# Optimization experiments

Hardware: AMD Instinct MI355X
Metric: run time of the kernel (lower is better)

Reference implementation:

```python
import jax, jax.numpy as jnp
import numpy as np

D_MODEL = 512
B, T = 2, 4096
LN_EPS = 1e-5


def _layernorm(x, gamma, beta):
    mu = jnp.mean(x, axis=-1, keepdims=True)
    var = jnp.mean((x - mu) ** 2, axis=-1, keepdims=True)
    return (x - mu) * jax.lax.rsqrt(var + LN_EPS) * gamma + beta


def setup_inputs() -> dict:
    key = jax.random.key(0)
    ks = jax.random.split(key, 16)
    d = D_MODEL
    s = 1.0 / np.sqrt(d)
    inp = {
        "tokens": jax.random.normal(ks[0], (B, T, d), dtype=jnp.float32),
        "Wq": jax.random.normal(ks[1], (d, d), dtype=jnp.float32) * s,
        "bq": jnp.zeros((d,), jnp.float32),
        "Wk": jax.random.normal(ks[2], (d, d), dtype=jnp.float32) * s,
        "bk": jnp.zeros((d,), jnp.float32),
        "Wv": jax.random.normal(ks[3], (d, d), dtype=jnp.float32) * s,
        "bv": jnp.zeros((d,), jnp.float32),
        "distance_scale": jnp.asarray(0.01, jnp.float32),
        "W1": jax.random.normal(ks[4], (d, 4 * d), dtype=jnp.float32) * s,
        "b1": jnp.zeros((4 * d,), jnp.float32),
        "W2": jax.random.normal(ks[5], (4 * d, d), dtype=jnp.float32) * (1.0 / np.sqrt(4 * d)),
        "b2": jnp.zeros((d,), jnp.float32),
        "g1": jnp.ones((d,), jnp.float32),
        "be1": jnp.zeros((d,), jnp.float32),
        "g2": jnp.ones((d,), jnp.float32),
        "be2": jnp.zeros((d,), jnp.float32),
    }
    return inp


def reference(tokens, Wq, bq, Wk, bk, Wv, bv, distance_scale,
              W1, b1, W2, b2, g1, be1, g2, be2):
    Bv, Tv, d = tokens.shape
    q = tokens @ Wq + bq
    k = tokens @ Wk + bk
    v = tokens @ Wv + bv
    # [B, T, T] raw scores
    scores = jnp.einsum('btd,bsd->bts', q, k)
    pos = jnp.arange(Tv)
    distance = jnp.abs(pos[None, :] - pos[:, None]).astype(jnp.float32)  # [T, T]
    scores = scores + (-distance_scale * distance)[None, :, :]
    causal = pos[None, :] > pos[:, None]  # strict upper triangle
    scores = jnp.where(causal[None, :, :], -jnp.inf, scores)
    scores = scores / jnp.sqrt(jnp.asarray(d, jnp.float32))
    attn = jax.nn.softmax(scores, axis=-1)
    attn_out = jnp.einsum('bts,bsd->btd', attn, v)
    x = _layernorm(tokens + attn_out, g1, be1)
    y = jnp.maximum(x @ W1 + b1, 0.0) @ W2 + b2
    z = _layernorm(y + x, g2, be2)
    return z
```

## Files before the change

kernel.cpp:

```cpp
#include <hip/hip_runtime.h>
#include <hip/hip_bf16.h>
#include <math.h>

typedef unsigned short u16;
typedef __attribute__((ext_vector_type(8))) short short8;
typedef __attribute__((ext_vector_type(4))) float float4v;

#define MFMA_BF16(a, b, c) __builtin_amdgcn_mfma_f32_16x16x32_bf16((a), (b), (c), 0, 0, 0)

typedef const __attribute__((address_space(1))) void* gas_ptr;
typedef __attribute__((address_space(3))) void* las_ptr;

__device__ __forceinline__ u16 f2bf(float f) {
  __hip_bfloat16 h = __float2bfloat16(f);
  return __builtin_bit_cast(u16, h);
}

__device__ __forceinline__ float bf2f(u16 v) {
  return __builtin_bit_cast(float, (unsigned)v << 16);
}

__device__ __forceinline__ void load_lds16(const u16* g, u16* l) {
  __builtin_amdgcn_global_load_lds((gas_ptr)g, (las_ptr)l, 16, 0, 0);
}

__device__ __forceinline__ void gemm_mainloop(
    const u16* __restrict__ A, const u16* __restrict__ Bt,
    int kb, int kend, int lda, int ldb,
    int m0, int n0, u16* As, u16* Bs, float4v acc[4][4])
{
  const int tid = threadIdx.x;
  const int w = tid >> 6, lane = tid & 63;
  const int wr = w >> 1, wc = w & 1;
  const int lr = lane & 15, lk = (lane >> 4) * 8;
  for (int k0 = kb; k0 < kend; k0 += 32) {
#pragma unroll
    for (int c = 0; c < 2; ++c) {
      int idx = c * 256 + w * 64 + lane;
      int r = idx >> 2, c8 = idx & 3;
      load_lds16(A + (size_t)(m0 + r) * lda + k0 + c8 * 8, As + (size_t)(c * 256 + w * 64) * 8);
      load_lds16(Bt + (size_t)(n0 + r) * ldb + k0 + c8 * 8, Bs + (size_t)(c * 256 + w * 64) * 8);
    }
    __syncthreads();
    short8 af[4], bf[4];
#pragma unroll
    for (int mt = 0; mt < 4; ++mt)
      af[mt] = *(const short8*)&As[(wr * 64 + mt * 16 + lr) * 32 + lk];
#pragma unroll
    for (int nt = 0; nt < 4; ++nt)
      bf[nt] = *(const short8*)&Bs[(wc * 64 + nt * 16 + lr) * 32 + lk];
#pragma unroll
    for (int mt = 0; mt < 4; ++mt)
#pragma unroll
      for (int nt = 0; nt < 4; ++nt)
        acc[mt][nt] = MFMA_BF16(af[mt], bf[nt], acc[mt][nt]);
    __syncthreads();
  }
}

__global__ __launch_bounds__(256) void gemm_qkv(
    const u16* __restrict__ A, const u16* __restrict__ Bt,
    const float* __restrict__ bq, const float* __restrict__ bk, const float* __restrict__ bv,
    u16* __restrict__ qo, u16* __restrict__ ko, u16* __restrict__ vto)
{
  __shared__ u16 As[128 * 32], Bs[128 * 32];
  float4v acc[4][4];
#pragma unroll
  for (int mt = 0; mt < 4; ++mt)
#pragma unroll
    for (int nt = 0; nt < 4; ++nt) acc[mt][nt] = (float4v){0.f, 0.f, 0.f, 0.f};
  const int m0 = blockIdx.y * 128, n0 = blockIdx.x * 128;
  gemm_mainloop(A, Bt, 0, 512, 512, 512, m0, n0, As, Bs, acc);
  const int tid = threadIdx.x, w = tid >> 6, lane = tid & 63;
  const int wr = w >> 1, wc = w & 1, lr = lane & 15, lg = lane >> 4;
#pragma unroll
  for (int mt = 0; mt < 4; ++mt) {
#pragma unroll
    for (int nt = 0; nt < 4; ++nt) {
      int n = n0 + wc * 64 + nt * 16 + lr;
#pragma unroll
      for (int r = 0; r < 4; ++r) {
        int i = m0 + wr * 64 + mt * 16 + lg * 4 + r;
        float v = acc[mt][nt][r];
        if (n < 512) {
          qo[(size_t)i * 512 + n] = f2bf(v + bq[n]);
        } else if (n < 1024) {
          ko[(size_t)i * 512 + (n - 512)] = f2bf(v + bk[n - 512]);
        } else {
          int bb = i >> 12, t = i & 4095;
          vto[((size_t)(bb * 512 + (n - 1024))) * 4096 + t] = f2bf(v + bv[n - 1024]);
        }
      }
    }
  }
}

__global__ __launch_bounds__(256) void gemm_qk_p(
    const u16* __restrict__ q, const u16* __restrict__ k,
    const float* __restrict__ dsp,
    u16* __restrict__ P, float* __restrict__ l)
{
  __shared__ u16 As[128 * 32], Bs[128 * 32];
  float4v acc[4][4];
#pragma unroll
  for (int mt = 0; mt < 4; ++mt)
#pragma unroll
    for (int nt = 0; nt < 4; ++nt) acc[mt][nt] = (float4v){0.f, 0.f, 0.f, 0.f};
  int idx = blockIdx.x;
  int tm = (int)((sqrtf(8.0f * (float)idx + 1.0f) - 1.0f) * 0.5f);
  while ((tm + 1) * (tm + 2) / 2 <= idx) ++tm;
  while (tm * (tm + 1) / 2 > idx) --tm;
  int tn = idx - tm * (tm + 1) / 2;
  const int m0 = tm * 128, n0 = tn * 128;
  gemm_mainloop(q, k, 0, 512, 512, 512, m0, n0, As, Bs, acc);
  const int tid = threadIdx.x, w = tid >> 6, lane = tid & 63;
  const int wr = w >> 1, wc = w & 1, lr = lane & 15, lg = lane >> 4;
  const float invs = 0.04419417382415922f;
  const float dsi = dsp[0] * invs;
  const float L2E = 1.4426950408889634f;
  float rs[4][4];
#pragma unroll
  for (int mt = 0; mt < 4; ++mt)
#pragma unroll
    for (int r = 0; r < 4; ++r) rs[mt][r] = 0.f;
#pragma unroll
  for (int mt = 0; mt < 4; ++mt) {
#pragma unroll
    for (int nt = 0; nt < 4; ++nt) {
      int j = n0 + wc * 64 + nt * 16 + lr;
#pragma unroll
      for (int r = 0; r < 4; ++r) {
        int i = m0 + wr * 64 + mt * 16 + lg * 4 + r;
        float x = acc[mt][nt][r] * invs - dsi * fabsf((float)(i - j));
        float p = (j > i) ? 0.f : exp2f(x * L2E);
        P[(size_t)i * 4096 + j] = f2bf(p);
        rs[mt][r] += p;
      }
    }
  }
#pragma unroll
  for (int mt = 0; mt < 4; ++mt) {
#pragma unroll
    for (int r = 0; r < 4; ++r) {
      float v = rs[mt][r];
#pragma unroll
      for (int off = 1; off < 16; off <<= 1) v += __shfl_xor(v, off, 64);
      if (lr == 0)
        atomicAdd(&l[m0 + wr * 64 + mt * 16 + lg * 4 + r], v);
    }
  }
}

__global__ __launch_bounds__(256) void gemm_pv(
    const u16* __restrict__ P, const u16* __restrict__ vt,
    float* __restrict__ of)
{
  __shared__ u16 As[128 * 32], Bs[128 * 32];
  float4v acc[4][4];
#pragma unroll
  for (int mt = 0; mt < 4; ++mt)
#pragma unroll
    for (int nt = 0; nt < 4; ++nt) acc[mt][nt] = (float4v){0.f, 0.f, 0.f, 0.f};
  int rem = blockIdx.y;
  int tm = 0, cpt = 1;
  while (rem >= cpt) { rem -= cpt; ++tm; cpt = (tm >> 3) + 1; }
  const int m0 = tm * 128, n0 = blockIdx.x * 128;
  const int kb = rem * 1024;
  const int kfull = (tm + 1) * 128;
  const int kend = (kb + 1024 < kfull) ? (kb + 1024) : kfull;
  gemm_mainloop(P, vt, kb, kend, 4096, 4096, m0, n0, As, Bs, acc);
  const int tid = threadIdx.x, w = tid >> 6, lane = tid & 63;
  const int wr = w >> 1, wc = w & 1, lr = lane & 15, lg = lane >> 4;
#pragma unroll
  for (int mt = 0; mt < 4; ++mt) {
#pragma unroll
    for (int nt = 0; nt < 4; ++nt) {
      int n = n0 + wc * 64 + nt * 16 + lr;
#pragma unroll
      for (int r = 0; r < 4; ++r) {
        int i = m0 + wr * 64 + mt * 16 + lg * 4 + r;
        atomicAdd(&of[(size_t)i * 512 + n], acc[mt][nt][r]);
      }
    }
  }
}

__global__ __launch_bounds__(256) void gemm_ffn1(
    const u16* __restrict__ A, const u16* __restrict__ Bt,
    const float* __restrict__ b1, u16* __restrict__ h)
{
  __shared__ u16 As[128 * 32], Bs[128 * 32];
  float4v acc[4][4];
#pragma unroll
  for (int mt = 0; mt < 4; ++mt)
#pragma unroll
    for (int nt = 0; nt < 4; ++nt) acc[mt][nt] = (float4v){0.f, 0.f, 0.f, 0.f};
  const int m0 = blockIdx.y * 128, n0 = blockIdx.x * 128;
  gemm_mainloop(A, Bt, 0, 512, 512, 512, m0, n0, As, Bs, acc);
  const int tid = threadIdx.x, w = tid >> 6, lane = tid & 63;
  const int wr = w >> 1, wc = w & 1, lr = lane & 15, lg = lane >> 4;
#pragma unroll
  for (int mt = 0; mt < 4; ++mt) {
#pragma unroll
    for (int nt = 0; nt < 4; ++nt) {
      int n = n0 + wc * 64 + nt * 16 + lr;
#pragma unroll
      for (int r = 0; r < 4; ++r) {
        int i = m0 + wr * 64 + mt * 16 + lg * 4 + r;
        h[(size_t)i * 2048 + n] = f2bf(fmaxf(acc[mt][nt][r] + b1[n], 0.f));
      }
    }
  }
}

__global__ __launch_bounds__(256) void gemm_ffn2(
    const u16* __restrict__ A, const u16* __restrict__ Bt,
    float* __restrict__ y0, u16* __restrict__ y1)
{
  __shared__ u16 As[128 * 32], Bs[128 * 32];
  float4v acc[4][4];
#pragma unroll
  for (int mt = 0; mt < 4; ++mt)
#pragma unroll
    for (int nt = 0; nt < 4; ++nt) acc[mt][nt] = (float4v){0.f, 0.f, 0.f, 0.f};
  const int m0 = blockIdx.y * 128, n0 = blockIdx.x * 128;
  const int kb = blockIdx.z * 1024;
  gemm_mainloop(A, Bt, kb, kb + 1024, 2048, 2048, m0, n0, As, Bs, acc);
  const int tid = threadIdx.x, w = tid >> 6, lane = tid & 63;
  const int wr = w >> 1, wc = w & 1, lr = lane & 15, lg = lane >> 4;
#pragma unroll
  for (int mt = 0; mt < 4; ++mt) {
#pragma unroll
    for (int nt = 0; nt < 4; ++nt) {
      int n = n0 + wc * 64 + nt * 16 + lr;
#pragma unroll
      for (int r = 0; r < 4; ++r) {
        int i = m0 + wr * 64 + mt * 16 + lg * 4 + r;
        if (blockIdx.z == 0) y0[(size_t)i * 512 + n] = acc[mt][nt][r];
        else                 y1[(size_t)i * 512 + n] = f2bf(acc[mt][nt][r]);
      }
    }
  }
}

__global__ __launch_bounds__(256) void ln1_kernel(
    const float* __restrict__ a, const float* __restrict__ lsum,
    const float* __restrict__ tok,
    const float* __restrict__ g, const float* __restrict__ be,
    float* __restrict__ of, u16* __restrict__ ob)
{
  const int row = blockIdx.x * 4 + (threadIdx.x >> 6);
  const int lane = threadIdx.x & 63;
  const size_t base = (size_t)row * 512 + lane * 8;
  const float linv = 1.0f / lsum[row];
  float v[8];
#pragma unroll
  for (int t = 0; t < 8; ++t)
    v[t] = a[base + t] * linv + tok[base + t];
  float s = 0.f;
#pragma unroll
  for (int t = 0; t < 8; ++t) s += v[t];
#pragma unroll
  for (int off = 1; off < 64; off <<= 1) s += __shfl_xor(s, off, 64);
  const float mu = s * (1.0f / 512.0f);
  float qv = 0.f;
#pragma unroll
  for (int t = 0; t < 8; ++t) { float d = v[t] - mu; qv += d * d; }
#pragma unroll
  for (int off = 1; off < 64; off <<= 1) qv += __shfl_xor(qv, off, 64);
  const float rs = rsqrtf(qv * (1.0f / 512.0f) + 1e-5f);
  const int cb = lane * 8;
#pragma unroll
  for (int t = 0; t < 8; ++t) {
    float xv = (v[t] - mu) * rs * g[cb + t] + be[cb + t];
    of[base + t] = xv;
    ob[base + t] = f2bf(xv);
  }
}

__global__ __launch_bounds__(256) void ln2_kernel(
    const float* __restrict__ y0, const u16* __restrict__ y1,
    const float* __restrict__ b2, const float* __restrict__ bsrc,
    const float* __restrict__ g, const float* __restrict__ be,
    float* __restrict__ of)
{
  const int row = blockIdx.x * 4 + (threadIdx.x >> 6);
  const int lane = threadIdx.x & 63;
  const size_t base = (size_t)row * 512 + lane * 8;
  const int cb = lane * 8;
  float v[8];
#pragma unroll
  for (int t = 0; t < 8; ++t)
    v[t] = y0[base + t] + bf2f(y1[base + t]) + b2[cb + t] + bsrc[base + t];
  float s = 0.f;
#pragma unroll
  for (int t = 0; t < 8; ++t) s += v[t];
#pragma unroll
  for (int off = 1; off < 64; off <<= 1) s += __shfl_xor(s, off, 64);
  const float mu = s * (1.0f / 512.0f);
  float qv = 0.f;
#pragma unroll
  for (int t = 0; t < 8; ++t) { float d = v[t] - mu; qv += d * d; }
#pragma unroll
  for (int off = 1; off < 64; off <<= 1) qv += __shfl_xor(qv, off, 64);
  const float rs = rsqrtf(qv * (1.0f / 512.0f) + 1e-5f);
#pragma unroll
  for (int t = 0; t < 8; ++t) {
    float xv = (v[t] - mu) * rs * g[cb + t] + be[cb + t];
    of[base + t] = xv;
  }
}

__global__ __launch_bounds__(256) void cast_bf_kernel(
    const float* __restrict__ in, u16* __restrict__ out)
{
  const size_t i = ((size_t)blockIdx.x * 256 + threadIdx.x) * 8;
#pragma unroll
  for (int t = 0; t < 8; ++t) out[i + t] = f2bf(in[i + t]);
}

__global__ __launch_bounds__(256) void transpose_qkv_kernel(
    const float* __restrict__ Wq, const float* __restrict__ Wk,
    const float* __restrict__ Wv, u16* __restrict__ dst)
{
  __shared__ u16 tile[32][33];
  const float* src = (blockIdx.z == 0) ? Wq : (blockIdx.z == 1) ? Wk : Wv;
  u16* d = dst + (size_t)blockIdx.z * 512 * 512;
  const int tx = threadIdx.x & 31, ty = threadIdx.x >> 5;
  const int n0 = blockIdx.x * 32, k0 = blockIdx.y * 32;
#pragma unroll
  for (int i = 0; i < 32; i += 8)
    tile[ty + i][tx] = f2bf(src[(size_t)(k0 + ty + i) * 512 + n0 + tx]);
  __syncthreads();
#pragma unroll
  for (int i = 0; i < 32; i += 8)
    d[(size_t)(n0 + ty + i) * 512 + k0 + tx] = tile[tx][ty + i];
}

__global__ __launch_bounds__(256) void transpose_bf_kernel(
    const float* __restrict__ src, u16* __restrict__ dst, int K, int N)
{
  __shared__ u16 tile[32][33];
  const int tx = threadIdx.x & 31, ty = threadIdx.x >> 5;
  const int n0 = blockIdx.x * 32, k0 = blockIdx.y * 32;
#pragma unroll
  for (int i = 0; i < 32; i += 8)
    tile[ty + i][tx] = f2bf(src[(size_t)(k0 + ty + i) * N + n0 + tx]);
  __syncthreads();
#pragma unroll
  for (int i = 0; i < 32; i += 8)
    dst[(size_t)(n0 + ty + i) * K + k0 + tx] = tile[tx][ty + i];
}

extern "C" void kernel_launch(void* const* d_in, const int* in_sizes, int n_in,
                              void* d_out, int out_size, void* d_ws, size_t ws_size,
                              hipStream_t stream) {
  const float* tokens = (const float*)d_in[0];
  const float* Wq = (const float*)d_in[1];
  const float* bq = (const float*)d_in[2];
  const float* Wk = (const float*)d_in[3];
  const float* bk = (const float*)d_in[4];
  const float* Wv = (const float*)d_in[5];
  const float* bv = (const float*)d_in[6];
  const float* dscale = (const float*)d_in[7];
  const float* W1 = (const float*)d_in[8];
  const float* b1 = (const float*)d_in[9];
  const float* W2 = (const float*)d_in[10];
  const float* b2 = (const float*)d_in[11];
  const float* g1 = (const float*)d_in[12];
  const float* be1 = (const float*)d_in[13];
  const float* g2 = (const float*)d_in[14];
  const float* be2 = (const float*)d_in[15];
  float* out = (float*)d_out;

  char* ws = (char*)d_ws;
  u16*   tok_bf = (u16*)(ws + 0);
  u16*   y1buf  = (u16*)(ws + 0);
  u16*   wqkvT  = (u16*)(ws + 8388608);
  u16*   w1T    = (u16*)(ws + 9961472);
  u16*   w2T    = (u16*)(ws + 12058624);
  u16*   qbuf   = (u16*)(ws + 14155776);
  u16*   kbuf   = (u16*)(ws + 22544384);
  u16*   vtbuf  = (u16*)(ws + 30932992);
  float* xf     = (float*)(ws + 14155776);
  u16*   xbf    = (u16*)(ws + 30932992);
  float* attnb  = (float*)(ws + 39321600);
  float* y0buf  = (float*)(ws + 39321600);
  u16*   Pbuf   = (u16*)(ws + 56098816);
  u16*   hbuf   = (u16*)(ws + 56098816);
  float* lbuf   = (float*)(ws + 89653248);

  (void)hipMemsetAsync(lbuf, 0, 2 * 4096 * sizeof(float), stream);
  (void)hipMemsetAsync(attnb, 0, (size_t)8192 * 512 * sizeof(float), stream);

  cast_bf_kernel<<<2048, 256, 0, stream>>>(tokens, tok_bf);
  transpose_qkv_kernel<<<dim3(16, 16, 3), 256, 0, stream>>>(Wq, Wk, Wv, wqkvT);
  transpose_bf_kernel<<<dim3(64, 16), 256, 0, stream>>>(W1, w1T, 512, 2048);
  transpose_bf_kernel<<<dim3(16, 64), 256, 0, stream>>>(W2, w2T, 2048, 512);

  gemm_qkv<<<dim3(12, 64), 256, 0, stream>>>(tok_bf, wqkvT, bq, bk, bv, qbuf, kbuf, vtbuf);

  for (int b = 0; b < 2; ++b) {
    const u16* qb = qbuf + (size_t)b * 4096 * 512;
    const u16* kb = kbuf + (size_t)b * 4096 * 512;
    const u16* vb = vtbuf + (size_t)b * 512 * 4096;
    gemm_qk_p<<<528, 256, 0, stream>>>(qb, kb, dscale, Pbuf, lbuf + b * 4096);
    gemm_pv<<<dim3(4, 80), 256, 0, stream>>>(Pbuf, vb, attnb + (size_t)b * 4096 * 512);
  }

  ln1_kernel<<<2048, 256, 0, stream>>>(attnb, lbuf, tokens, g1, be1, xf, xbf);

  gemm_ffn1<<<dim3(16, 64), 256, 0, stream>>>(xbf, w1T, b1, hbuf);

  gemm_ffn2<<<dim3(4, 64, 2), 256, 0, stream>>>(hbuf, w2T, y0buf, y1buf);

  ln2_kernel<<<2048, 256, 0, stream>>>(y0buf, y1buf, b2, xf, g2, be2, out);
}
```

Baseline: 352.2 us.

## Batch attention kernels across both batches and replace PV atomics with split-K partial buffers

The per-batch loop of QK/P and PV launches becomes single launches using a grid dimension for the batch, so each kernel gets twice as many blocks and two launches disappear. The P buffer now holds both batches. The PV kernel no longer does float atomicAdd into a zeroed accumulator. Each K-split writes its partial result to its own buffer (fp32 for the first split, bf16 for the rest), and ln1 sums the four partials. This trades atomic traffic for extra buffers, a larger workspace, bf16 rounding of the partial sums, and a memset over the three bf16 partial buffers.

```diff
diff --git a/kernel.cpp b/kernel.cpp
--- a/kernel.cpp
+++ b/kernel.cpp
@@ -106,13 +106,18 @@
   for (int mt = 0; mt < 4; ++mt)
 #pragma unroll
     for (int nt = 0; nt < 4; ++nt) acc[mt][nt] = (float4v){0.f, 0.f, 0.f, 0.f};
+  const int b = blockIdx.y;
+  const u16* qb = q + (size_t)b * 4096 * 512;
+  const u16* kb = k + (size_t)b * 4096 * 512;
+  u16* Pb = P + (size_t)b * 4096 * 4096;
+  float* lb = l + b * 4096;
   int idx = blockIdx.x;
   int tm = (int)((sqrtf(8.0f * (float)idx + 1.0f) - 1.0f) * 0.5f);
   while ((tm + 1) * (tm + 2) / 2 <= idx) ++tm;
   while (tm * (tm + 1) / 2 > idx) --tm;
   int tn = idx - tm * (tm + 1) / 2;
   const int m0 = tm * 128, n0 = tn * 128;
-  gemm_mainloop(q, k, 0, 512, 512, 512, m0, n0, As, Bs, acc);
+  gemm_mainloop(qb, kb, 0, 512, 512, 512, m0, n0, As, Bs, acc);
   const int tid = threadIdx.x, w = tid >> 6, lane = tid & 63;
   const int wr = w >> 1, wc = w & 1, lr = lane & 15, lg = lane >> 4;
   const float invs = 0.04419417382415922f;
@@ -133,7 +138,7 @@
         int i = m0 + wr * 64 + mt * 16 + lg * 4 + r;
         float x = acc[mt][nt][r] * invs - dsi * fabsf((float)(i - j));
         float p = (j > i) ? 0.f : exp2f(x * L2E);
-        P[(size_t)i * 4096 + j] = f2bf(p);
+        Pb[(size_t)i * 4096 + j] = f2bf(p);
         rs[mt][r] += p;
       }
     }
@@ -146,14 +151,15 @@
 #pragma unroll
       for (int off = 1; off < 16; off <<= 1) v += __shfl_xor(v, off, 64);
       if (lr == 0)
-        atomicAdd(&l[m0 + wr * 64 + mt * 16 + lg * 4 + r], v);
+        atomicAdd(&lb[m0 + wr * 64 + mt * 16 + lg * 4 + r], v);
     }
   }
 }
 
 __global__ __launch_bounds__(256) void gemm_pv(
     const u16* __restrict__ P, const u16* __restrict__ vt,
-    float* __restrict__ of)
+    float* __restrict__ y0, u16* __restrict__ y1,
+    u16* __restrict__ y2, u16* __restrict__ y3)
 {
   __shared__ u16 As[128 * 32], Bs[128 * 32];
   float4v acc[4][4];
@@ -161,6 +167,9 @@
   for (int mt = 0; mt < 4; ++mt)
 #pragma unroll
     for (int nt = 0; nt < 4; ++nt) acc[mt][nt] = (float4v){0.f, 0.f, 0.f, 0.f};
+  const int b = blockIdx.z;
+  const u16* Pb = P + (size_t)b * 4096 * 4096;
+  const u16* vb = vt + (size_t)b * 512 * 4096;
   int rem = blockIdx.y;
   int tm = 0, cpt = 1;
   while (rem >= cpt) { rem -= cpt; ++tm; cpt = (tm >> 3) + 1; }
@@ -168,9 +177,10 @@
   const int kb = rem * 1024;
   const int kfull = (tm + 1) * 128;
   const int kend = (kb + 1024 < kfull) ? (kb + 1024) : kfull;
-  gemm_mainloop(P, vt, kb, kend, 4096, 4096, m0, n0, As, Bs, acc);
+  gemm_mainloop(Pb, vb, kb, kend, 4096, 4096, m0, n0, As, Bs, acc);
   const int tid = threadIdx.x, w = tid >> 6, lane = tid & 63;
   const int wr = w >> 1, wc = w & 1, lr = lane & 15, lg = lane >> 4;
+  const size_t bofs = (size_t)b * 4096 * 512;
 #pragma unroll
   for (int mt = 0; mt < 4; ++mt) {
 #pragma unroll
@@ -179,7 +189,12 @@
 #pragma unroll
       for (int r = 0; r < 4; ++r) {
         int i = m0 + wr * 64 + mt * 16 + lg * 4 + r;
-        atomicAdd(&of[(size_t)i * 512 + n], acc[mt][nt][r]);
+        size_t o = bofs + (size_t)i * 512 + n;
+        float v = acc[mt][nt][r];
+        if (rem == 0)      y0[o] = v;
+        else if (rem == 1) y1[o] = f2bf(v);
+        else if (rem == 2) y2[o] = f2bf(v);
+        else               y3[o] = f2bf(v);
       }
     }
   }
@@ -215,7 +230,7 @@
 
 __global__ __launch_bounds__(256) void gemm_ffn2(
     const u16* __restrict__ A, const u16* __restrict__ Bt,
-    float* __restrict__ y0, u16* __restrict__ y1)
+    float* __restrict__ f0, u16* __restrict__ f1)
 {
   __shared__ u16 As[128 * 32], Bs[128 * 32];
   float4v acc[4][4];
@@ -236,16 +251,17 @@
 #pragma unroll
       for (int r = 0; r < 4; ++r) {
         int i = m0 + wr * 64 + mt * 16 + lg * 4 + r;
-        if (blockIdx.z == 0) y0[(size_t)i * 512 + n] = acc[mt][nt][r];
-        else                 y1[(size_t)i * 512 + n] = f2bf(acc[mt][nt][r]);
+        if (blockIdx.z == 0) f0[(size_t)i * 512 + n] = acc[mt][nt][r];
+        else                 f1[(size_t)i * 512 + n] = f2bf(acc[mt][nt][r]);
       }
     }
   }
 }
 
 __global__ __launch_bounds__(256) void ln1_kernel(
-    const float* __restrict__ a, const float* __restrict__ lsum,
-    const float* __restrict__ tok,
+    const float* __restrict__ y0, const u16* __restrict__ y1,
+    const u16* __restrict__ y2, const u16* __restrict__ y3,
+    const float* __restrict__ lsum, const float* __restrict__ tok,
     const float* __restrict__ g, const float* __restrict__ be,
     float* __restrict__ of, u16* __restrict__ ob)
 {
@@ -255,8 +271,10 @@
   const float linv = 1.0f / lsum[row];
   float v[8];
 #pragma unroll
-  for (int t = 0; t < 8; ++t)
-    v[t] = a[base + t] * linv + tok[base + t];
+  for (int t = 0; t < 8; ++t) {
+    float a = y0[base + t] + bf2f(y1[base + t]) + bf2f(y2[base + t]) + bf2f(y3[base + t]);
+    v[t] = a * linv + tok[base + t];
+  }
   float s = 0.f;
 #pragma unroll
   for (int t = 0; t < 8; ++t) s += v[t];
@@ -279,7 +297,7 @@
 }
 
 __global__ __launch_bounds__(256) void ln2_kernel(
-    const float* __restrict__ y0, const u16* __restrict__ y1,
+    const float* __restrict__ f0, const u16* __restrict__ f1,
     const float* __restrict__ b2, const float* __restrict__ bsrc,
     const float* __restrict__ g, const float* __restrict__ be,
     float* __restrict__ of)
@@ -291,7 +309,7 @@
   float v[8];
 #pragma unroll
   for (int t = 0; t < 8; ++t)
-    v[t] = y0[base + t] + bf2f(y1[base + t]) + b2[cb + t] + bsrc[base + t];
+    v[t] = f0[base + t] + bf2f(f1[base + t]) + b2[cb + t] + bsrc[base + t];
   float s = 0.f;
 #pragma unroll
   for (int t = 0; t < 8; ++t) s += v[t];
@@ -375,23 +393,26 @@
 
   char* ws = (char*)d_ws;
   u16*   tok_bf = (u16*)(ws + 0);
-  u16*   y1buf  = (u16*)(ws + 0);
   u16*   wqkvT  = (u16*)(ws + 8388608);
   u16*   w1T    = (u16*)(ws + 9961472);
   u16*   w2T    = (u16*)(ws + 12058624);
   u16*   qbuf   = (u16*)(ws + 14155776);
   u16*   kbuf   = (u16*)(ws + 22544384);
   u16*   vtbuf  = (u16*)(ws + 30932992);
-  float* xf     = (float*)(ws + 14155776);
-  u16*   xbf    = (u16*)(ws + 30932992);
-  float* attnb  = (float*)(ws + 39321600);
-  float* y0buf  = (float*)(ws + 39321600);
-  u16*   Pbuf   = (u16*)(ws + 56098816);
-  u16*   hbuf   = (u16*)(ws + 56098816);
-  float* lbuf   = (float*)(ws + 89653248);
+  u16*   Pbuf   = (u16*)(ws + 39321600);
+  float* y0buf  = (float*)(ws + 106430464);
+  u16*   y1buf  = (u16*)(ws + 123207680);
+  u16*   y2buf  = (u16*)(ws + 131596288);
+  u16*   y3buf  = (u16*)(ws + 139984896);
+  float* xf     = (float*)(ws + 148373504);
+  u16*   xbf    = (u16*)(ws + 165150720);
+  u16*   hbuf   = (u16*)(ws + 173539328);
+  float* f0buf  = (float*)(ws + 207093760);
+  u16*   f1buf  = (u16*)(ws + 223870976);
+  float* lbuf   = (float*)(ws + 232259584);
 
   (void)hipMemsetAsync(lbuf, 0, 2 * 4096 * sizeof(float), stream);
-  (void)hipMemsetAsync(attnb, 0, (size_t)8192 * 512 * sizeof(float), stream);
+  (void)hipMemsetAsync(y1buf, 0, (size_t)3 * 8388608, stream);
 
   cast_bf_kernel<<<2048, 256, 0, stream>>>(tokens, tok_bf);
   transpose_qkv_kernel<<<dim3(16, 16, 3), 256, 0, stream>>>(Wq, Wk, Wv, wqkvT);
@@ -400,19 +421,15 @@
 
   gemm_qkv<<<dim3(12, 64), 256, 0, stream>>>(tok_bf, wqkvT, bq, bk, bv, qbuf, kbuf, vtbuf);
 
-  for (int b = 0; b < 2; ++b) {
-    const u16* qb = qbuf + (size_t)b * 4096 * 512;
-    const u16* kb = kbuf + (size_t)b * 4096 * 512;
-    const u16* vb = vtbuf + (size_t)b * 512 * 4096;
-    gemm_qk_p<<<528, 256, 0, stream>>>(qb, kb, dscale, Pbuf, lbuf + b * 4096);
-    gemm_pv<<<dim3(4, 80), 256, 0, stream>>>(Pbuf, vb, attnb + (size_t)b * 4096 * 512);
-  }
-
-  ln1_kernel<<<2048, 256, 0, stream>>>(attnb, lbuf, tokens, g1, be1, xf, xbf);
+  gemm_qk_p<<<dim3(528, 2), 256, 0, stream>>>(qbuf, kbuf, dscale, Pbuf, lbuf);
+  gemm_pv<<<dim3(4, 80, 2), 256, 0, stream>>>(Pbuf, vtbuf, y0buf, y1buf, y2buf, y3buf);
+
+  ln1_kernel<<<2048, 256, 0, stream>>>(y0buf, y1buf, y2buf, y3buf, lbuf, tokens,
+                                       g1, be1, xf, xbf);
 
   gemm_ffn1<<<dim3(16, 64), 256, 0, stream>>>(xbf, w1T, b1, hbuf);
 
-  gemm_ffn2<<<dim3(4, 64, 2), 256, 0, stream>>>(hbuf, w2T, y0buf, y1buf);
-
-  ln2_kernel<<<2048, 256, 0, stream>>>(y0buf, y1buf, b2, xf, g2, be2, out);
-}
+  gemm_ffn2<<<dim3(4, 64, 2), 256, 0, stream>>>(hbuf, w2T, f0buf, f1buf);
+
+  ln2_kernel<<<2048, 256, 0, stream>>>(f0buf, f1buf, b2, xf, g2, be2, out);
+}
```

Result: faster. 326.2 us (-7.4%).
